# Kernel tuning notes

Hardware: AMD Instinct MI355X
Metric: run time of the kernel (lower is better)

## Reference

```python
import jax, jax.numpy as jnp
import numpy as np

N_NODES = 50000
N_RAND_EDGES = 500000
IN_FEATS = 128
HIDDEN = 512
N_IDS = 4096


def setup_inputs() -> dict:
    key = jax.random.key(0)
    k1, k2, k3, k4, k5, k6 = jax.random.split(key, 6)
    feat = jax.random.normal(k1, (N_NODES, IN_FEATS), dtype=jnp.float32)
    W_neigh = jax.random.normal(k2, (HIDDEN, IN_FEATS), dtype=jnp.float32) * (1.0 / np.sqrt(IN_FEATS))
    bias = jnp.zeros((HIDDEN,), dtype=jnp.float32)
    self_loop = jnp.arange(N_NODES, dtype=jnp.int64 if jax.config.jax_enable_x64 else jnp.int32)
    src = jnp.concatenate([jax.random.randint(k3, (N_RAND_EDGES,), 0, N_NODES), self_loop])
    dst = jnp.concatenate([jax.random.randint(k4, (N_RAND_EDGES,), 0, N_NODES), self_loop])
    ids = jax.random.randint(k5, (N_IDS,), 0, N_NODES)
    return {"feat": feat, "W_neigh": W_neigh, "bias": bias, "src": src, "dst": dst, "ids": ids}


def reference(feat, W_neigh, bias, src, dst, ids):
    # DGL SAGEConv, aggregator_type='gcn' (graph includes self-loops):
    #   neigh_sum[v] = sum_{(u->v)} feat[u]
    #   h_neigh[v] = (neigh_sum[v] + feat[v]) / (in_deg(v) + 1)
    #   rst = fc_neigh(h_neigh) + bias
    # SageEmbedder applies no per-layer activation (single layer), then tanh.
    N = feat.shape[0]
    neigh_sum = jax.ops.segment_sum(feat[src], dst, num_segments=N)  # [N, F]
    deg = jax.ops.segment_sum(jnp.ones_like(dst, dtype=feat.dtype), dst, num_segments=N)  # [N]
    h_neigh = (neigh_sum + feat) / (deg[:, None] + 1.0)
    h = jnp.tanh(h_neigh @ W_neigh.T + bias)  # [N, H]
    return h[ids]  # [B, H] id -> node embedding lookup
```

## Files before the change

kernel.cpp:

```cpp
#include <hip/hip_runtime.h>
#include <math.h>

#define N_NODES 50000
#define IN_F    128
#define HIDDEN  512
#define N_IDS   4096
#define CAP     64

__global__ void k_mark(const int* __restrict__ ids, int* __restrict__ slot,
                       int* __restrict__ cursor) {
    int i = blockIdx.x * blockDim.x + threadIdx.x;
    if (i < N_IDS) { slot[ids[i]] = i; cursor[i] = 0; }
}

__global__ __launch_bounds__(256) void k_edges(
        const int4* __restrict__ src4, const int4* __restrict__ dst4, int n4,
        const int* __restrict__ src, const int* __restrict__ dst, int n_edges,
        const int* __restrict__ slot, int* __restrict__ cursor,
        int* __restrict__ wl2) {
    int i = blockIdx.x * 256 + threadIdx.x;
    int stride = gridDim.x * 256;
    for (int q = i; q < n4; q += stride) {
        int4 d = dst4[q];
        int s0 = slot[d.x], s1 = slot[d.y], s2 = slot[d.z], s3 = slot[d.w];
        if ((s0 >= 0) | (s1 >= 0) | (s2 >= 0) | (s3 >= 0)) {
            int4 u = src4[q];
            if (s0 >= 0) { int p = atomicAdd(&cursor[s0], 1); if (p < CAP) wl2[(s0 << 6) + p] = u.x; }
            if (s1 >= 0) { int p = atomicAdd(&cursor[s1], 1); if (p < CAP) wl2[(s1 << 6) + p] = u.y; }
            if (s2 >= 0) { int p = atomicAdd(&cursor[s2], 1); if (p < CAP) wl2[(s2 << 6) + p] = u.z; }
            if (s3 >= 0) { int p = atomicAdd(&cursor[s3], 1); if (p < CAP) wl2[(s3 << 6) + p] = u.w; }
        }
    }
    for (int e = n4 * 4 + i; e < n_edges; e += stride) {
        int s = slot[dst[e]];
        if (s >= 0) { int p = atomicAdd(&cursor[s], 1); if (p < CAP) wl2[(s << 6) + p] = src[e]; }
    }
}

__global__ __launch_bounds__(256) void k_agg(
        const int* __restrict__ ids, const int* __restrict__ slot,
        const int* __restrict__ cursor, const int* __restrict__ wl2,
        const float4* __restrict__ feat4, float4* __restrict__ h4) {
    const int g    = threadIdx.x >> 5;
    const int lane = threadIdx.x & 31;
    const int s    = blockIdx.x * 8 + g;
    const int v    = ids[s];
    if (slot[v] != s) return;
    const int d  = cursor[s];
    const int dc = min(d, CAP);
    float4 acc = feat4[(size_t)v * (IN_F / 4) + lane];
    for (int e = 0; e < dc; ++e) {
        int u = wl2[(s << 6) + e];
        float4 x = feat4[(size_t)u * (IN_F / 4) + lane];
        acc.x += x.x; acc.y += x.y; acc.z += x.z; acc.w += x.w;
    }
    float inv = 1.0f / (float)(d + 1);
    acc.x *= inv; acc.y *= inv; acc.z *= inv; acc.w *= inv;
    h4[(size_t)s * (IN_F / 4) + lane] = acc;
}

#define IDS_PER_BLOCK 16

__global__ __launch_bounds__(256) void k_gemm(
    const int* __restrict__ ids, const int* __restrict__ slot,
    const float* __restrict__ h, const float* __restrict__ W,
    const float* __restrict__ bias, float* __restrict__ out) {
    const int i0 = blockIdx.x * IDS_PER_BLOCK;
    const int t  = threadIdx.x;

    int sli[IDS_PER_BLOCK];
#pragma unroll
    for (int li = 0; li < IDS_PER_BLOCK; ++li)
        sli[li] = __builtin_amdgcn_readfirstlane(slot[ids[i0 + li]]);

    const float4* W4 = (const float4*)W;
    const float4* H4 = (const float4*)h;
    float acc0[IDS_PER_BLOCK], acc1[IDS_PER_BLOCK];
#pragma unroll
    for (int li = 0; li < IDS_PER_BLOCK; ++li) { acc0[li] = 0.0f; acc1[li] = 0.0f; }

    const int j0 = t, j1 = t + 256;
    for (int k4 = 0; k4 < IN_F / 4; ++k4) {
        float4 w0 = W4[(size_t)j0 * (IN_F / 4) + k4];
        float4 w1 = W4[(size_t)j1 * (IN_F / 4) + k4];
#pragma unroll
        for (int li = 0; li < IDS_PER_BLOCK; ++li) {
            float4 hv = H4[(size_t)sli[li] * (IN_F / 4) + k4];
            acc0[li] += w0.x * hv.x + w0.y * hv.y + w0.z * hv.z + w0.w * hv.w;
            acc1[li] += w1.x * hv.x + w1.y * hv.y + w1.z * hv.z + w1.w * hv.w;
        }
    }

    float b0 = bias[j0], b1 = bias[j1];
#pragma unroll
    for (int li = 0; li < IDS_PER_BLOCK; ++li) {
        size_t row = (size_t)(i0 + li) * HIDDEN;
        out[row + j0] = tanhf(acc0[li] + b0);
        out[row + j1] = tanhf(acc1[li] + b1);
    }
}

extern "C" void kernel_launch(void* const* d_in, const int* in_sizes, int n_in,
                              void* d_out, int out_size, void* d_ws, size_t ws_size,
                              hipStream_t stream) {
    const float* feat  = (const float*)d_in[0];
    const float* W     = (const float*)d_in[1];
    const float* bias  = (const float*)d_in[2];
    const int*   src   = (const int*)d_in[3];
    const int*   dst   = (const int*)d_in[4];
    const int*   ids   = (const int*)d_in[5];
    float*       out   = (float*)d_out;
    const int n_edges  = in_sizes[3];
    const int n4       = n_edges / 4;

    char* ws = (char*)d_ws;
    size_t off = 0;
    int*   slot   = (int*)(ws + off);   off += ((size_t)N_NODES * 4 + 1023) & ~1023ull;
    float* h      = (float*)(ws + off); off += (size_t)N_IDS * IN_F * 4;
    int*   cursor = (int*)(ws + off);   off += (size_t)N_IDS * 4;
    int*   wl2    = (int*)(ws + off);   off += (size_t)N_IDS * CAP * 4;

    k_mark<<<(N_IDS + 255) / 256, 256, 0, stream>>>(ids, slot, cursor);
    k_edges<<<(n4 + 255) / 256, 256, 0, stream>>>((const int4*)src, (const int4*)dst, n4,
                                                  src, dst, n_edges, slot, cursor, wl2);
    k_agg<<<N_IDS / 8, 256, 0, stream>>>(ids, slot, cursor, wl2,
                                         (const float4*)feat, (float4*)h);
    k_gemm<<<N_IDS / IDS_PER_BLOCK, 256, 0, stream>>>(ids, slot, h, W, bias, out);
}
```

Measured before the change: 130.5 us.

## Fuse mark, edge scan and aggregation into one cooperative kernel

Merges the slot marking, edge bucketing and neighbor aggregation kernels into one cooperative kernel of 512 blocks, separated by grid-wide syncs. This removes two kernel launches and their inter-kernel gaps. The aggregated rows are now written per id index instead of per slot, so the GEMM indexes h directly without the slot indirection. Duplicate ids now each compute their own aggregation instead of skipping. The edge scan now runs as a grid-stride loop over fewer threads, and the grid syncs add their own overhead.

```diff
diff --git a/kernel.cpp b/kernel.cpp
--- a/kernel.cpp
+++ b/kernel.cpp
@@ -1,5 +1,8 @@
 #include <hip/hip_runtime.h>
+#include <hip/hip_cooperative_groups.h>
 #include <math.h>
+
+namespace cg = cooperative_groups;
 
 #define N_NODES 50000
 #define IN_F    128
@@ -7,20 +10,23 @@
 #define N_IDS   4096
 #define CAP     64
 
-__global__ void k_mark(const int* __restrict__ ids, int* __restrict__ slot,
-                       int* __restrict__ cursor) {
-    int i = blockIdx.x * blockDim.x + threadIdx.x;
-    if (i < N_IDS) { slot[ids[i]] = i; cursor[i] = 0; }
-}
+#define COOP_BLOCKS  512
+#define COOP_THREADS 256
 
-__global__ __launch_bounds__(256) void k_edges(
+__global__ __launch_bounds__(COOP_THREADS) void k_front(
+        const int* __restrict__ ids, int* __restrict__ slot, int* __restrict__ cursor,
         const int4* __restrict__ src4, const int4* __restrict__ dst4, int n4,
         const int* __restrict__ src, const int* __restrict__ dst, int n_edges,
-        const int* __restrict__ slot, int* __restrict__ cursor,
-        int* __restrict__ wl2) {
-    int i = blockIdx.x * 256 + threadIdx.x;
-    int stride = gridDim.x * 256;
-    for (int q = i; q < n4; q += stride) {
+        int* __restrict__ wl2, const float4* __restrict__ feat4,
+        float4* __restrict__ h4) {
+    cg::grid_group grid = cg::this_grid();
+    const int tid = blockIdx.x * COOP_THREADS + threadIdx.x;
+    const int nthreads = COOP_BLOCKS * COOP_THREADS;
+
+    if (tid < N_IDS) { slot[ids[tid]] = tid; cursor[tid] = 0; }
+    grid.sync();
+
+    for (int q = tid; q < n4; q += nthreads) {
         int4 d = dst4[q];
         int s0 = slot[d.x], s1 = slot[d.y], s2 = slot[d.z], s3 = slot[d.w];
         if ((s0 >= 0) | (s1 >= 0) | (s2 >= 0) | (s3 >= 0)) {
@@ -31,23 +37,19 @@
             if (s3 >= 0) { int p = atomicAdd(&cursor[s3], 1); if (p < CAP) wl2[(s3 << 6) + p] = u.w; }
         }
     }
-    for (int e = n4 * 4 + i; e < n_edges; e += stride) {
+    for (int e = n4 * 4 + tid; e < n_edges; e += nthreads) {
         int s = slot[dst[e]];
         if (s >= 0) { int p = atomicAdd(&cursor[s], 1); if (p < CAP) wl2[(s << 6) + p] = src[e]; }
     }
-}
+    grid.sync();
 
-__global__ __launch_bounds__(256) void k_agg(
-        const int* __restrict__ ids, const int* __restrict__ slot,
-        const int* __restrict__ cursor, const int* __restrict__ wl2,
-        const float4* __restrict__ feat4, float4* __restrict__ h4) {
     const int g    = threadIdx.x >> 5;
     const int lane = threadIdx.x & 31;
-    const int s    = blockIdx.x * 8 + g;
-    const int v    = ids[s];
-    if (slot[v] != s) return;
-    const int d  = cursor[s];
-    const int dc = min(d, CAP);
+    const int i    = blockIdx.x * 8 + g;
+    const int v    = ids[i];
+    const int s    = slot[v];
+    const int d    = cursor[s];
+    const int dc   = min(d, CAP);
     float4 acc = feat4[(size_t)v * (IN_F / 4) + lane];
     for (int e = 0; e < dc; ++e) {
         int u = wl2[(s << 6) + e];
@@ -56,22 +58,16 @@
     }
     float inv = 1.0f / (float)(d + 1);
     acc.x *= inv; acc.y *= inv; acc.z *= inv; acc.w *= inv;
-    h4[(size_t)s * (IN_F / 4) + lane] = acc;
+    h4[(size_t)i * (IN_F / 4) + lane] = acc;
 }
 
 #define IDS_PER_BLOCK 16
 
 __global__ __launch_bounds__(256) void k_gemm(
-    const int* __restrict__ ids, const int* __restrict__ slot,
-    const float* __restrict__ h, const float* __restrict__ W,
-    const float* __restrict__ bias, float* __restrict__ out) {
+        const float* __restrict__ h, const float* __restrict__ W,
+        const float* __restrict__ bias, float* __restrict__ out) {
     const int i0 = blockIdx.x * IDS_PER_BLOCK;
     const int t  = threadIdx.x;
-
-    int sli[IDS_PER_BLOCK];
-#pragma unroll
-    for (int li = 0; li < IDS_PER_BLOCK; ++li)
-        sli[li] = __builtin_amdgcn_readfirstlane(slot[ids[i0 + li]]);
 
     const float4* W4 = (const float4*)W;
     const float4* H4 = (const float4*)h;
@@ -85,7 +81,7 @@
         float4 w1 = W4[(size_t)j1 * (IN_F / 4) + k4];
 #pragma unroll
         for (int li = 0; li < IDS_PER_BLOCK; ++li) {
-            float4 hv = H4[(size_t)sli[li] * (IN_F / 4) + k4];
+            float4 hv = H4[(size_t)(i0 + li) * (IN_F / 4) + k4];
             acc0[li] += w0.x * hv.x + w0.y * hv.y + w0.z * hv.z + w0.w * hv.w;
             acc1[li] += w1.x * hv.x + w1.y * hv.y + w1.z * hv.z + w1.w * hv.w;
         }
@@ -110,8 +106,8 @@
     const int*   dst   = (const int*)d_in[4];
     const int*   ids   = (const int*)d_in[5];
     float*       out   = (float*)d_out;
-    const int n_edges  = in_sizes[3];
-    const int n4       = n_edges / 4;
+    int          n_edges = in_sizes[3];
+    int          n4      = n_edges / 4;
 
     char* ws = (char*)d_ws;
     size_t off = 0;
@@ -120,10 +116,16 @@
     int*   cursor = (int*)(ws + off);   off += (size_t)N_IDS * 4;
     int*   wl2    = (int*)(ws + off);   off += (size_t)N_IDS * CAP * 4;
 
-    k_mark<<<(N_IDS + 255) / 256, 256, 0, stream>>>(ids, slot, cursor);
-    k_edges<<<(n4 + 255) / 256, 256, 0, stream>>>((const int4*)src, (const int4*)dst, n4,
-                                                  src, dst, n_edges, slot, cursor, wl2);
-    k_agg<<<N_IDS / 8, 256, 0, stream>>>(ids, slot, cursor, wl2,
-                                         (const float4*)feat, (float4*)h);
-    k_gemm<<<N_IDS / IDS_PER_BLOCK, 256, 0, stream>>>(ids, slot, h, W, bias, out);
+    const int4* src4 = (const int4*)src;
+    const int4* dst4 = (const int4*)dst;
+    float4*     h4   = (float4*)h;
+    const float4* feat4 = (const float4*)feat;
+
+    void* args[] = { (void*)&ids, (void*)&slot, (void*)&cursor,
+                     (void*)&src4, (void*)&dst4, (void*)&n4,
+                     (void*)&src, (void*)&dst, (void*)&n_edges,
+                     (void*)&wl2, (void*)&feat4, (void*)&h4 };
+    hipLaunchCooperativeKernel((const void*)k_front, dim3(COOP_BLOCKS),
+                               dim3(COOP_THREADS), args, 0, stream);
+    k_gemm<<<N_IDS / IDS_PER_BLOCK, 256, 0, stream>>>(h, W, bias, out);
 }
```

Result: slower. 234.6 us (+79.8%).
